# Kernel optimization log

Hardware: AMD Instinct MI355X
Metric: run time of the kernel (lower is better)

The kernel has to match this reference:

```python
import jax, jax.numpy as jnp
import numpy as np

D_MODEL = 1024
NHEAD = 16
HEAD_DIM = D_MODEL // NHEAD
EPS = 1e-5


def _layer_norm(x, gamma, beta):
    mu = jnp.mean(x, axis=-1, keepdims=True)
    var = jnp.mean(jnp.square(x - mu), axis=-1, keepdims=True)
    return (x - mu) * jax.lax.rsqrt(var + EPS) * gamma + beta


def setup_inputs() -> dict:
    key = jax.random.key(0)
    ks = jax.random.split(key, 8)
    s = 1.0 / np.sqrt(D_MODEL)
    return {
        "x": jax.random.normal(ks[0], (4, 2048, D_MODEL), dtype=jnp.float32),
        "Wq": jax.random.uniform(ks[1], (D_MODEL, D_MODEL), jnp.float32, -s, s),
        "Wk": jax.random.uniform(ks[2], (D_MODEL, D_MODEL), jnp.float32, -s, s),
        "Wv": jax.random.uniform(ks[3], (D_MODEL, D_MODEL), jnp.float32, -s, s),
        "ln1_g": jnp.ones((D_MODEL,), jnp.float32),
        "ln1_b": jnp.zeros((D_MODEL,), jnp.float32),
        "ln2_g": jnp.ones((D_MODEL,), jnp.float32),
        "ln2_b": jnp.zeros((D_MODEL,), jnp.float32),
        "W1": jax.random.uniform(ks[4], (D_MODEL, D_MODEL), jnp.float32, -s, s),
        "b1": jax.random.uniform(ks[5], (D_MODEL,), jnp.float32, -s, s),
        "W2": jax.random.uniform(ks[6], (D_MODEL, D_MODEL), jnp.float32, -s, s),
        "b2": jax.random.uniform(ks[7], (D_MODEL,), jnp.float32, -s, s),
    }


def reference(x, Wq, Wk, Wv, ln1_g, ln1_b, ln2_g, ln2_b, W1, b1, W2, b2):
    B, S, D = x.shape
    temperature = jnp.sqrt(jnp.asarray(D_MODEL / NHEAD, x.dtype))
    xn = _layer_norm(x, ln1_g, ln1_b)
    # torch Linear: y = x @ W.T (weights are [out, in], no bias for q/k/v)
    q = (xn @ Wq.T).reshape(B, S, NHEAD, HEAD_DIM)
    k = (xn @ Wk.T).reshape(B, S, NHEAD, HEAD_DIM)
    v = (xn @ Wv.T).reshape(B, S, NHEAD, HEAD_DIM)
    scores = jnp.einsum("bqhd,bkhd->bhqk", q, k) / temperature  # [B,H,S,S]
    causal = jnp.tril(jnp.ones((S, S), dtype=bool))
    scores = jnp.where(causal, scores, jnp.asarray(-jnp.inf, scores.dtype))
    attn = jax.nn.softmax(scores, axis=-1)
    att_out = jnp.einsum("bhqk,bkhd->bqhd", attn, v).reshape(B, S, D)
    xt = x + att_out
    xt2 = _layer_norm(xt, ln2_g, ln2_b)
    ffn = jax.nn.relu(xt2 @ W1.T + b1) @ W2.T + b2  # dropout=0 -> identity
    return xt + ffn
```

## Files before the change

### kernel.cpp

```cpp
#include <hip/hip_runtime.h>
#include <hip/hip_bf16.h>

typedef unsigned short u16;
typedef unsigned int u32;
typedef __attribute__((ext_vector_type(8))) __bf16 bf16x8;
typedef __attribute__((ext_vector_type(4))) float f32x4;
typedef __attribute__((ext_vector_type(8))) unsigned short ushort8v;
typedef __attribute__((ext_vector_type(4))) unsigned short u16x4;
typedef __attribute__((ext_vector_type(2))) unsigned int u32x2;

#define DEV __device__ __forceinline__
#define AS1 __attribute__((address_space(1)))
#define AS3 __attribute__((address_space(3)))

DEV u16 f2bf(float f) {
    union { float f; unsigned int i; } u; u.f = f;
    unsigned int x = u.i;
    unsigned int r = (x + 0x7fffu + ((x >> 16) & 1u)) >> 16;
    return (u16)r;
}
DEV float bf2f(u16 h) {
    union { unsigned int i; float f; } u; u.i = ((unsigned int)h) << 16;
    return u.f;
}
DEV u32 cvt_pk_bf16(float lo, float hi) {
    u32 r;
    asm("v_cvt_pk_bf16_f32 %0, %1, %2" : "=v"(r) : "v"(lo), "v"(hi));
    return r;
}

__global__ __launch_bounds__(256) void cvt_w(
    const float* __restrict__ wq, const float* __restrict__ wk,
    const float* __restrict__ wv, const float* __restrict__ w1,
    const float* __restrict__ w2, u16* __restrict__ dst)
{
    const int i = (blockIdx.x * 256 + threadIdx.x) * 4;
    if (i >= (1 << 20)) return;
    auto conv4 = [](float4 a) {
        u16x4 r; r[0] = f2bf(a.x); r[1] = f2bf(a.y); r[2] = f2bf(a.z); r[3] = f2bf(a.w);
        return r;
    };
    *(u16x4*)(dst + i)               = conv4(*(const float4*)(wq + i));
    *(u16x4*)(dst + (1 << 20) + i)   = conv4(*(const float4*)(wk + i));
    *(u16x4*)(dst + (2 << 20) + i)   = conv4(*(const float4*)(wv + i));
    *(u16x4*)(dst + (3 << 20) + i)   = conv4(*(const float4*)(w1 + i));
    *(u16x4*)(dst + (4 << 20) + i)   = conv4(*(const float4*)(w2 + i));
}

template<bool ADD>
__global__ __launch_bounds__(256) void ln_kernel(
    const float* __restrict__ xin, const u16* __restrict__ addbf,
    const float* __restrict__ g, const float* __restrict__ be,
    float* __restrict__ xt_out, u16* __restrict__ y_bf)
{
    const int row = blockIdx.x;
    const int tid = threadIdx.x;
    const size_t base = (size_t)row * 1024 + tid * 4;

    float4 xv = *(const float4*)(xin + base);
    float v[4] = {xv.x, xv.y, xv.z, xv.w};
    if (ADD) {
        u16x4 a = *(const u16x4*)(addbf + base);
        v[0] += bf2f(a[0]); v[1] += bf2f(a[1]); v[2] += bf2f(a[2]); v[3] += bf2f(a[3]);
        float4 o; o.x = v[0]; o.y = v[1]; o.z = v[2]; o.w = v[3];
        *(float4*)(xt_out + base) = o;
    }
    float s = 0.f, ss = 0.f;
    #pragma unroll
    for (int j = 0; j < 4; ++j) { s += v[j]; ss += v[j] * v[j]; }
    #pragma unroll
    for (int o = 32; o > 0; o >>= 1) { s += __shfl_xor(s, o); ss += __shfl_xor(ss, o); }
    __shared__ float red[8];
    const int w = tid >> 6;
    if ((tid & 63) == 0) { red[w * 2] = s; red[w * 2 + 1] = ss; }
    __syncthreads();
    s  = red[0] + red[2] + red[4] + red[6];
    ss = red[1] + red[3] + red[5] + red[7];
    const float mu = s * (1.0f / 1024.0f);
    const float var = ss * (1.0f / 1024.0f) - mu * mu;
    const float rstd = rsqrtf(var + 1e-5f);

    const int col = tid * 4;
    float4 gv = *(const float4*)(g + col);
    float4 bv = *(const float4*)(be + col);
    u16x4 o4;
    o4[0] = f2bf((v[0] - mu) * rstd * gv.x + bv.x);
    o4[1] = f2bf((v[1] - mu) * rstd * gv.y + bv.y);
    o4[2] = f2bf((v[2] - mu) * rstd * gv.z + bv.z);
    o4[3] = f2bf((v[3] - mu) * rstd * gv.w + bv.w);
    *(u16x4*)(y_bf + base) = o4;
}

template<int EPI>
__global__ __launch_bounds__(256, 2) void gemm_bt(
    const u16* __restrict__ A, const u16* __restrict__ Bt,
    void* __restrict__ Cout, const float* __restrict__ bias,
    const float* __restrict__ resid, int M, int N, int K)
{
    __shared__ u16 As[2 * 128 * 32];
    __shared__ u16 Bs[2 * 128 * 32];
    const int tid = threadIdx.x;
    const int l = tid & 63;
    const int w = tid >> 6;
    const int wm = w >> 1, wn = w & 1;
    const int fr = l & 15, fc = l >> 4;
    const size_t rowA0 = (size_t)blockIdx.x * 128;
    const size_t rowB0 = (size_t)blockIdx.y * 128;

    f32x4 acc[4][4] = {};
    const int ldoff = fr * 32 + fc * 8;

    const int nkt = K >> 6;
    for (int kt = 0; kt < nkt; ++kt) {
        __syncthreads();
        const int k0 = kt << 6;
        #pragma unroll
        for (int q = 0; q < 4; ++q) {
            const int row = (q & 1) * 64 + w * 16 + (l >> 2);
            const int kk  = (q >> 1) * 32 + (l & 3) * 8;
            const u16* ga = A  + (rowA0 + row) * K + k0 + kk;
            const u16* gb = Bt + (rowB0 + row) * K + k0 + kk;
            u16* da = As + q * 2048 + w * 512;
            u16* db = Bs + q * 2048 + w * 512;
            __builtin_amdgcn_global_load_lds((const AS1 void*)ga, (AS3 void*)da, 16, 0, 0);
            __builtin_amdgcn_global_load_lds((const AS1 void*)gb, (AS3 void*)db, 16, 0, 0);
        }
        __syncthreads();
        #pragma unroll
        for (int ks = 0; ks < 2; ++ks) {
            const u16* as_p = As + ks * 4096;
            const u16* bs_p = Bs + ks * 4096;
            bf16x8 af[4], bfv[4];
            #pragma unroll
            for (int m = 0; m < 4; ++m)
                af[m] = *(const bf16x8*)(as_p + (wm * 64 + m * 16) * 32 + ldoff);
            #pragma unroll
            for (int n = 0; n < 4; ++n)
                bfv[n] = *(const bf16x8*)(bs_p + (wn * 64 + n * 16) * 32 + ldoff);
            #pragma unroll
            for (int m = 0; m < 4; ++m)
                #pragma unroll
                for (int n = 0; n < 4; ++n)
                    acc[m][n] = __builtin_amdgcn_mfma_f32_16x16x32_bf16(
                        af[m], bfv[n], acc[m][n], 0, 0, 0);
        }
    }

    const int r0 = (int)rowA0 + wm * 64;
    const int c0 = (int)rowB0 + wn * 64;
    #pragma unroll
    for (int m = 0; m < 4; ++m) {
        #pragma unroll
        for (int n = 0; n < 4; ++n) {
            const int row = r0 + m * 16 + fc * 4;
            const int col = c0 + n * 16 + fr;
            #pragma unroll
            for (int j = 0; j < 4; ++j) {
                float v = acc[m][n][j];
                if constexpr (EPI == 0) {
                    const int rowj = row + j;
                    const int which = col >> 10;
                    const int hh = (col >> 6) & 15;
                    const int dd = col & 63;
                    const size_t dst = (size_t)which * 8388608 +
                        ((((size_t)(rowj >> 11) * 16 + hh) * 2048 + (rowj & 2047)) * 64 + dd);
                    ((u16*)Cout)[dst] = f2bf(v);
                } else if constexpr (EPI == 1) {
                    const size_t idx = (size_t)(row + j) * N + col;
                    v += bias[col];
                    v = fmaxf(v, 0.0f);
                    ((u16*)Cout)[idx] = f2bf(v);
                } else {
                    const size_t idx = (size_t)(row + j) * N + col;
                    v += bias[col] + resid[idx];
                    ((float*)Cout)[idx] = v;
                }
            }
        }
    }
}

__global__ __launch_bounds__(256, 4) void attn_fwd(
    const u16* __restrict__ Qh, const u16* __restrict__ Kh,
    const u16* __restrict__ Vh, u16* __restrict__ attout)
{
    __shared__ u16 Ks[2][64 * 64];
    __shared__ u16 Vt[2][64 * 64];
    __shared__ u16 Pw[4 * 16 * 64];

    const int bid = blockIdx.x;
    const int pair = (bid >> 3) & 15;
    const int g = (bid & 7) + 8 * (bid >> 7);
    const int h = g & 15, b = g >> 4;

    const int tid = threadIdx.x, l = tid & 63, w = tid >> 6;
    const int fr = l & 15, fc = l >> 4;
    const int hb = b * 16 + h;
    const size_t head = (size_t)hb << 17;
    const u16* kb_g = Kh + head;
    const u16* vb_g = Vh + head;
    u16* pw = Pw + w * 1024;

    const int sw = (fr & 7) << 3;
    const int col0 = (fc * 8) ^ sw;
    const int col1 = col0 ^ 32;

    const int krow0 = w * 16 + (l >> 3);
    const int kdsw  = ((l & 7) * 8) ^ ((l >> 3) << 3);

    const int kr = tid >> 2;
    const int kc0 = (tid & 3) * 16;

    const float qs = 0.125f * 1.44269504f;

    bf16x8 onesv;
    #pragma unroll
    for (int j = 0; j < 8; ++j) onesv[j] = (__bf16)1.0f;

    #pragma unroll 1
    for (int half = 0; half < 2; ++half) {
        const int qt = half ? 31 - pair : pair;
        const int qbase = qt * 64 + w * 16;
        const int qg = qbase + fr;

        const u16* qp = Qh + head + (size_t)(qbase + fr) * 64 + fc * 8;
        bf16x8 qf0 = *(const bf16x8*)qp;
        bf16x8 qf1 = *(const bf16x8*)(qp + 32);
        #pragma unroll
        for (int j = 0; j < 8; ++j) {
            qf0[j] = (__bf16)((float)qf0[j] * qs);
            qf1[j] = (__bf16)((float)qf1[j] * qs);
        }

        f32x4 acc_o[4] = {};
        float m_run = -3.0e38f;
        float l_run[4] = {0.f, 0.f, 0.f, 0.f};

        const int nkt = qt + 1;
        int cur = 0;

        #pragma unroll
        for (int i = 0; i < 2; ++i) {
            const int row = krow0 + i * 8;
            __builtin_amdgcn_global_load_lds(
                (const AS1 void*)(kb_g + (size_t)row * 64 + kdsw),
                (AS3 void*)(&Ks[0][0] + (w * 16 + i * 8) * 64), 16, 0, 0);
        }
        __builtin_amdgcn_sched_barrier(0);
        {
            ushort8v v0a = *(const ushort8v*)(vb_g + (size_t)kr * 64 + kc0);
            ushort8v v0b = *(const ushort8v*)(vb_g + (size_t)kr * 64 + kc0 + 8);
            #pragma unroll
            for (int j = 0; j < 8; ++j) {
                const int d0 = kc0 + j, d1 = kc0 + 8 + j;
                Vt[0][d0 * 64 + (kr ^ ((d0 & 7) << 3) ^ ((d0 >> 4) << 4))] = v0a[j];
                Vt[0][d1 * 64 + (kr ^ ((d1 & 7) << 3) ^ ((d1 >> 4) << 4))] = v0b[j];
            }
        }
        ushort8v vA, vB;
        if (nkt > 1) {
            vA = *(const ushort8v*)(vb_g + (size_t)(64 + kr) * 64 + kc0);
            vB = *(const ushort8v*)(vb_g + (size_t)(64 + kr) * 64 + kc0 + 8);
        }
        __builtin_amdgcn_sched_barrier(0);
        if (nkt > 1) asm volatile("s_waitcnt vmcnt(2)" ::: "memory");
        else         asm volatile("s_waitcnt vmcnt(0)" ::: "memory");
        asm volatile("s_waitcnt lgkmcnt(0)" ::: "memory");
        __builtin_amdgcn_s_barrier();

        #pragma unroll 1
        for (int kt = 0; kt < nkt; ++kt) {
            const int kv0 = kt * 64;
            const bool diag = (kt == qt);
            const u16* ksc = &Ks[cur][0];
            const u16* vtc = &Vt[cur][0];

            if (kt + 1 < nkt) {
                u16* ksn = &Ks[cur ^ 1][0];
                #pragma unroll
                for (int i = 0; i < 2; ++i) {
                    const int row = krow0 + i * 8;
                    __builtin_amdgcn_global_load_lds(
                        (const AS1 void*)(kb_g + (size_t)(kv0 + 64 + row) * 64 + kdsw),
                        (AS3 void*)(ksn + (w * 16 + i * 8) * 64), 16, 0, 0);
                }
            }
            __builtin_amdgcn_sched_barrier(0);

            f32x4 sa[4] = {};
            __builtin_amdgcn_s_setprio(1);
            #pragma unroll
            for (int nb = 0; nb < 4; ++nb) {
                const u16* kb = ksc + (nb * 16 + fr) * 64;
                sa[nb] = __builtin_amdgcn_mfma_f32_16x16x32_bf16(
                    *(const bf16x8*)(kb + col0), qf0, sa[nb], 0, 0, 0);
                sa[nb] = __builtin_amdgcn_mfma_f32_16x16x32_bf16(
                    *(const bf16x8*)(kb + col1), qf1, sa[nb], 0, 0, 0);
            }
            __builtin_amdgcn_s_setprio(0);

            if (diag) {
                #pragma unroll
                for (int nb = 0; nb < 4; ++nb)
                    #pragma unroll
                    for (int j = 0; j < 4; ++j) {
                        const int kg = kv0 + nb * 16 + fc * 4 + j;
                        if (kg > qg) sa[nb][j] = -3.0e38f;
                    }
            }

            float mx = sa[0][0];
            #pragma unroll
            for (int nb = 0; nb < 4; ++nb)
                #pragma unroll
                for (int j = 0; j < 4; ++j)
                    mx = fmaxf(mx, sa[nb][j]);
            mx = fmaxf(mx, __shfl_xor(mx, 16));
            mx = fmaxf(mx, __shfl_xor(mx, 32));

            if (__any(mx > m_run + 8.0f)) {
                const float mn = fmaxf(m_run, mx);
                const float alpha = exp2f(m_run - mn);
                m_run = mn;
                float aj[4];
                #pragma unroll
                for (int j = 0; j < 4; ++j)
                    aj[j] = __shfl(alpha, fc * 4 + j);
                #pragma unroll
                for (int j = 0; j < 4; ++j)
                    l_run[j] *= aj[j];
                #pragma unroll
                for (int db = 0; db < 4; ++db)
                    #pragma unroll
                    for (int j = 0; j < 4; ++j)
                        acc_o[db][j] *= aj[j];
            }

            #pragma unroll
            for (int nb = 0; nb < 4; ++nb)
                #pragma unroll
                for (int j = 0; j < 4; ++j)
                    sa[nb][j] = exp2f(sa[nb][j] - m_run);

            #pragma unroll
            for (int nb = 0; nb < 4; ++nb) {
                u32x2 pkv;
                pkv[0] = cvt_pk_bf16(sa[nb][0], sa[nb][1]);
                pkv[1] = cvt_pk_bf16(sa[nb][2], sa[nb][3]);
                *(u32x2*)(pw + fr * 64 + ((nb * 16 + fc * 4) ^ sw)) = pkv;
            }
            const u16* prd = pw + fr * 64;
            const bf16x8 pf0 = *(const bf16x8*)(prd + col0);
            const bf16x8 pf1 = *(const bf16x8*)(prd + col1);
            f32x4 acc_s = {};
            __builtin_amdgcn_s_setprio(1);
            #pragma unroll
            for (int db = 0; db < 4; ++db) {
                const u16* vb = vtc + (db * 16 + fr) * 64;
                const int vx = db << 4;
                acc_o[db] = __builtin_amdgcn_mfma_f32_16x16x32_bf16(
                    pf0, *(const bf16x8*)(vb + (col0 ^ vx)), acc_o[db], 0, 0, 0);
                acc_o[db] = __builtin_amdgcn_mfma_f32_16x16x32_bf16(
                    pf1, *(const bf16x8*)(vb + (col1 ^ vx)), acc_o[db], 0, 0, 0);
            }
            acc_s = __builtin_amdgcn_mfma_f32_16x16x32_bf16(pf0, onesv, acc_s, 0, 0, 0);
            acc_s = __builtin_amdgcn_mfma_f32_16x16x32_bf16(pf1, onesv, acc_s, 0, 0, 0);
            __builtin_amdgcn_s_setprio(0);
            #pragma unroll
            for (int j = 0; j < 4; ++j)
                l_run[j] += acc_s[j];

            if (kt + 1 < nkt) {
                u16* vtn = &Vt[cur ^ 1][0];
                #pragma unroll
                for (int j = 0; j < 8; ++j) {
                    const int d0 = kc0 + j, d1 = kc0 + 8 + j;
                    vtn[d0 * 64 + (kr ^ ((d0 & 7) << 3) ^ ((d0 >> 4) << 4))] = vA[j];
                    vtn[d1 * 64 + (kr ^ ((d1 & 7) << 3) ^ ((d1 >> 4) << 4))] = vB[j];
                }
            }
            if (kt + 2 < nkt) {
                const u16* vn = vb_g + (size_t)(kv0 + 128 + kr) * 64 + kc0;
                vA = *(const ushort8v*)vn;
                vB = *(const ushort8v*)(vn + 8);
            }
            __builtin_amdgcn_sched_barrier(0);
            if (kt + 1 < nkt) {
                if (kt + 2 < nkt) asm volatile("s_waitcnt vmcnt(2)" ::: "memory");
                else              asm volatile("s_waitcnt vmcnt(0)" ::: "memory");
            }
            asm volatile("s_waitcnt lgkmcnt(0)" ::: "memory");
            __builtin_amdgcn_s_barrier();
            cur ^= 1;
        }

        float inv[4];
        #pragma unroll
        for (int j = 0; j < 4; ++j) inv[j] = 1.0f / l_run[j];
        const size_t bS = (size_t)b * 2048;
        #pragma unroll
        for (int db = 0; db < 4; ++db)
            #pragma unroll
            for (int j = 0; j < 4; ++j)
                attout[(bS + qbase + fc * 4 + j) * 1024 + h * 64 + db * 16 + fr] =
                    f2bf(acc_o[db][j] * inv[j]);
    }
}

extern "C" void kernel_launch(void* const* d_in, const int* in_sizes, int n_in,
                              void* d_out, int out_size, void* d_ws, size_t ws_size,
                              hipStream_t stream)
{
    const float* x    = (const float*)d_in[0];
    const float* Wq   = (const float*)d_in[1];
    const float* Wk   = (const float*)d_in[2];
    const float* Wv   = (const float*)d_in[3];
    const float* ln1g = (const float*)d_in[4];
    const float* ln1b = (const float*)d_in[5];
    const float* ln2g = (const float*)d_in[6];
    const float* ln2b = (const float*)d_in[7];
    const float* W1   = (const float*)d_in[8];
    const float* b1   = (const float*)d_in[9];
    const float* W2   = (const float*)d_in[10];
    const float* b2   = (const float*)d_in[11];

    char* ws = (char*)d_ws;
    u16*   wbf  = (u16*)(ws);
    u16*   xn   = (u16*)(ws + 10485760);
    u16*   qkvb = (u16*)(ws + 27262976);
    u16*   attb = (u16*)(ws + 77594624);
    float* xt   = (float*)(ws + 94371840);

    cvt_w<<<1024, 256, 0, stream>>>(Wq, Wk, Wv, W1, W2, wbf);
    ln_kernel<false><<<8192, 256, 0, stream>>>(x, nullptr, ln1g, ln1b, nullptr, xn);
    gemm_bt<0><<<dim3(64, 24), 256, 0, stream>>>(xn, wbf, qkvb, nullptr, nullptr,
                                                 8192, 3072, 1024);
    attn_fwd<<<1024, 256, 0, stream>>>(qkvb, qkvb + 8388608, qkvb + 16777216, attb);
    ln_kernel<true><<<8192, 256, 0, stream>>>(x, attb, ln2g, ln2b, xt, xn);
    gemm_bt<1><<<dim3(64, 8), 256, 0, stream>>>(xn, wbf + (3 << 20), qkvb, b1, nullptr,
                                                8192, 1024, 1024);
    gemm_bt<2><<<dim3(64, 8), 256, 0, stream>>>(qkvb, wbf + (4 << 20), d_out, b2, xt,
                                                8192, 1024, 1024);
}
```

Before: 227.7 us.

## Enlarge attention query tile to 128 rows with two 16-row sub-tiles per wave

Each attention block now handles 128 query rows (32 per wave, as two 16-row MFMA sub-tiles) instead of 64. Every K/V tile loaded into LDS is therefore reused across twice as many queries, which halves K/V staging traffic and barrier count per query, and the grid shrinks to 512 blocks. Per-wave register use roughly doubles for accumulators, so launch bounds drop to 2 waves per SIMD. The coarser tiles also leave fewer blocks for load balancing, and waves whose rows end before the diagonal sit idle on some iterations.

```diff
diff --git a/kernel.cpp b/kernel.cpp
--- a/kernel.cpp
+++ b/kernel.cpp
@@ -180,17 +180,17 @@
     }
 }
 
-__global__ __launch_bounds__(256, 4) void attn_fwd(
+__global__ __launch_bounds__(256, 2) void attn_fwd(
     const u16* __restrict__ Qh, const u16* __restrict__ Kh,
     const u16* __restrict__ Vh, u16* __restrict__ attout)
 {
     __shared__ u16 Ks[2][64 * 64];
     __shared__ u16 Vt[2][64 * 64];
-    __shared__ u16 Pw[4 * 16 * 64];
+    __shared__ u16 Pw[4][32 * 64];
 
     const int bid = blockIdx.x;
-    const int pair = (bid >> 3) & 15;
-    const int g = (bid & 7) + 8 * (bid >> 7);
+    const int pair = (bid >> 3) & 7;
+    const int g = (bid & 7) + 8 * (bid >> 6);
     const int h = g & 15, b = g >> 4;
 
     const int tid = threadIdx.x, l = tid & 63, w = tid >> 6;
@@ -199,7 +199,7 @@
     const size_t head = (size_t)hb << 17;
     const u16* kb_g = Kh + head;
     const u16* vb_g = Vh + head;
-    u16* pw = Pw + w * 1024;
+    u16* pw = &Pw[w][0];
 
     const int sw = (fr & 7) << 3;
     const int col0 = (fc * 8) ^ sw;
@@ -219,24 +219,27 @@
 
     #pragma unroll 1
     for (int half = 0; half < 2; ++half) {
-        const int qt = half ? 31 - pair : pair;
-        const int qbase = qt * 64 + w * 16;
-        const int qg = qbase + fr;
-
-        const u16* qp = Qh + head + (size_t)(qbase + fr) * 64 + fc * 8;
-        bf16x8 qf0 = *(const bf16x8*)qp;
-        bf16x8 qf1 = *(const bf16x8*)(qp + 32);
-        #pragma unroll
-        for (int j = 0; j < 8; ++j) {
-            qf0[j] = (__bf16)((float)qf0[j] * qs);
-            qf1[j] = (__bf16)((float)qf1[j] * qs);
-        }
-
-        f32x4 acc_o[4] = {};
-        float m_run = -3.0e38f;
-        float l_run[4] = {0.f, 0.f, 0.f, 0.f};
-
-        const int nkt = qt + 1;
+        const int qt = half ? 15 - pair : pair;
+        const int qbw = qt * 128 + w * 32;
+
+        bf16x8 qf[2][2];
+        #pragma unroll
+        for (int qq = 0; qq < 2; ++qq) {
+            const u16* qp = Qh + head + (size_t)(qbw + qq * 16 + fr) * 64 + fc * 8;
+            qf[qq][0] = *(const bf16x8*)qp;
+            qf[qq][1] = *(const bf16x8*)(qp + 32);
+            #pragma unroll
+            for (int j = 0; j < 8; ++j) {
+                qf[qq][0][j] = (__bf16)((float)qf[qq][0][j] * qs);
+                qf[qq][1][j] = (__bf16)((float)qf[qq][1][j] * qs);
+            }
+        }
+
+        f32x4 acc_o[2][4] = {};
+        f32x4 l_run[2] = {};
+        float m_run[2] = {-3.0e38f, -3.0e38f};
+
+        const int nkt = 2 * qt + 2;
         int cur = 0;
 
         #pragma unroll
@@ -258,20 +261,18 @@
             }
         }
         ushort8v vA, vB;
-        if (nkt > 1) {
+        {
             vA = *(const ushort8v*)(vb_g + (size_t)(64 + kr) * 64 + kc0);
             vB = *(const ushort8v*)(vb_g + (size_t)(64 + kr) * 64 + kc0 + 8);
         }
         __builtin_amdgcn_sched_barrier(0);
-        if (nkt > 1) asm volatile("s_waitcnt vmcnt(2)" ::: "memory");
-        else         asm volatile("s_waitcnt vmcnt(0)" ::: "memory");
+        asm volatile("s_waitcnt vmcnt(2)" ::: "memory");
         asm volatile("s_waitcnt lgkmcnt(0)" ::: "memory");
         __builtin_amdgcn_s_barrier();
 
         #pragma unroll 1
         for (int kt = 0; kt < nkt; ++kt) {
             const int kv0 = kt * 64;
-            const bool diag = (kt == qt);
             const u16* ksc = &Ks[cur][0];
             const u16* vtc = &Vt[cur][0];
 
@@ -287,88 +288,124 @@
             }
             __builtin_amdgcn_sched_barrier(0);
 
-            f32x4 sa[4] = {};
-            __builtin_amdgcn_s_setprio(1);
-            #pragma unroll
-            for (int nb = 0; nb < 4; ++nb) {
-                const u16* kb = ksc + (nb * 16 + fr) * 64;
-                sa[nb] = __builtin_amdgcn_mfma_f32_16x16x32_bf16(
-                    *(const bf16x8*)(kb + col0), qf0, sa[nb], 0, 0, 0);
-                sa[nb] = __builtin_amdgcn_mfma_f32_16x16x32_bf16(
-                    *(const bf16x8*)(kb + col1), qf1, sa[nb], 0, 0, 0);
-            }
-            __builtin_amdgcn_s_setprio(0);
-
-            if (diag) {
-                #pragma unroll
-                for (int nb = 0; nb < 4; ++nb)
-                    #pragma unroll
-                    for (int j = 0; j < 4; ++j) {
-                        const int kg = kv0 + nb * 16 + fc * 4 + j;
-                        if (kg > qg) sa[nb][j] = -3.0e38f;
+            if (kv0 <= qbw + 31) {
+                f32x4 sa[2][4] = {};
+                __builtin_amdgcn_s_setprio(1);
+                #pragma unroll
+                for (int nb = 0; nb < 4; ++nb) {
+                    const u16* kb = ksc + (nb * 16 + fr) * 64;
+                    const bf16x8 kf0 = *(const bf16x8*)(kb + col0);
+                    const bf16x8 kf1 = *(const bf16x8*)(kb + col1);
+                    #pragma unroll
+                    for (int qq = 0; qq < 2; ++qq) {
+                        sa[qq][nb] = __builtin_amdgcn_mfma_f32_16x16x32_bf16(
+                            kf0, qf[qq][0], sa[qq][nb], 0, 0, 0);
+                        sa[qq][nb] = __builtin_amdgcn_mfma_f32_16x16x32_bf16(
+                            kf1, qf[qq][1], sa[qq][nb], 0, 0, 0);
                     }
-            }
-
-            float mx = sa[0][0];
-            #pragma unroll
-            for (int nb = 0; nb < 4; ++nb)
-                #pragma unroll
-                for (int j = 0; j < 4; ++j)
-                    mx = fmaxf(mx, sa[nb][j]);
-            mx = fmaxf(mx, __shfl_xor(mx, 16));
-            mx = fmaxf(mx, __shfl_xor(mx, 32));
-
-            if (__any(mx > m_run + 8.0f)) {
-                const float mn = fmaxf(m_run, mx);
-                const float alpha = exp2f(m_run - mn);
-                m_run = mn;
-                float aj[4];
-                #pragma unroll
-                for (int j = 0; j < 4; ++j)
-                    aj[j] = __shfl(alpha, fc * 4 + j);
-                #pragma unroll
-                for (int j = 0; j < 4; ++j)
-                    l_run[j] *= aj[j];
-                #pragma unroll
-                for (int db = 0; db < 4; ++db)
+                }
+                __builtin_amdgcn_s_setprio(0);
+
+                if (kv0 + 64 > qbw) {
+                    #pragma unroll
+                    for (int qq = 0; qq < 2; ++qq) {
+                        const int qg = qbw + qq * 16 + fr;
+                        #pragma unroll
+                        for (int nb = 0; nb < 4; ++nb)
+                            #pragma unroll
+                            for (int j = 0; j < 4; ++j) {
+                                const int kg = kv0 + nb * 16 + fc * 4 + j;
+                                if (kg > qg) sa[qq][nb][j] = -3.0e38f;
+                            }
+                    }
+                }
+
+                float mx[2];
+                #pragma unroll
+                for (int qq = 0; qq < 2; ++qq) {
+                    float m = sa[qq][0][0];
+                    #pragma unroll
+                    for (int nb = 0; nb < 4; ++nb)
+                        #pragma unroll
+                        for (int j = 0; j < 4; ++j)
+                            m = fmaxf(m, sa[qq][nb][j]);
+                    m = fmaxf(m, __shfl_xor(m, 16));
+                    m = fmaxf(m, __shfl_xor(m, 32));
+                    mx[qq] = m;
+                }
+
+                const bool need = (mx[0] > m_run[0] + 8.0f) || (mx[1] > m_run[1] + 8.0f);
+                if (__any(need)) {
+                    #pragma unroll
+                    for (int qq = 0; qq < 2; ++qq) {
+                        const float mn = fmaxf(m_run[qq], mx[qq]);
+                        const float alpha = exp2f(m_run[qq] - mn);
+                        m_run[qq] = mn;
+                        #pragma unroll
+                        for (int j = 0; j < 4; ++j) {
+                            const float aj = __shfl(alpha, fc * 4 + j);
+                            l_run[qq][j] *= aj;
+                            #pragma unroll
+                            for (int db = 0; db < 4; ++db)
+                                acc_o[qq][db][j] *= aj;
+                        }
+                    }
+                }
+
+                #pragma unroll
+                for (int qq = 0; qq < 2; ++qq)
+                    #pragma unroll
+                    for (int nb = 0; nb < 4; ++nb)
+                        #pragma unroll
+                        for (int j = 0; j < 4; ++j)
+                            sa[qq][nb][j] = exp2f(sa[qq][nb][j] - m_run[qq]);
+
+                #pragma unroll
+                for (int qq = 0; qq < 2; ++qq)
+                    #pragma unroll
+                    for (int nb = 0; nb < 4; ++nb) {
+                        u32x2 pkv;
+                        pkv[0] = cvt_pk_bf16(sa[qq][nb][0], sa[qq][nb][1]);
+                        pkv[1] = cvt_pk_bf16(sa[qq][nb][2], sa[qq][nb][3]);
+                        *(u32x2*)(pw + (qq * 16 + fr) * 64 + ((nb * 16 + fc * 4) ^ sw)) = pkv;
+                    }
+                bf16x8 pf[2][2];
+                #pragma unroll
+                for (int qq = 0; qq < 2; ++qq) {
+                    const u16* prd = pw + (qq * 16 + fr) * 64;
+                    pf[qq][0] = *(const bf16x8*)(prd + col0);
+                    pf[qq][1] = *(const bf16x8*)(prd + col1);
+                }
+                f32x4 acc_s[2] = {};
+                __builtin_amdgcn_s_setprio(1);
+                #pragma unroll
+                for (int db = 0; db < 4; ++db) {
+                    const u16* vb = vtc + (db * 16 + fr) * 64;
+                    const int vx = db << 4;
+                    const bf16x8 vf0 = *(const bf16x8*)(vb + (col0 ^ vx));
+                    const bf16x8 vf1 = *(const bf16x8*)(vb + (col1 ^ vx));
+                    #pragma unroll
+                    for (int qq = 0; qq < 2; ++qq) {
+                        acc_o[qq][db] = __builtin_amdgcn_mfma_f32_16x16x32_bf16(
+                            pf[qq][0], vf0, acc_o[qq][db], 0, 0, 0);
+                        acc_o[qq][db] = __builtin_amdgcn_mfma_f32_16x16x32_bf16(
+                            pf[qq][1], vf1, acc_o[qq][db], 0, 0, 0);
+                    }
+                }
+                #pragma unroll
+                for (int qq = 0; qq < 2; ++qq) {
+                    acc_s[qq] = __builtin_amdgcn_mfma_f32_16x16x32_bf16(
+                        pf[qq][0], onesv, acc_s[qq], 0, 0, 0);
+                    acc_s[qq] = __builtin_amdgcn_mfma_f32_16x16x32_bf16(
+                        pf[qq][1], onesv, acc_s[qq], 0, 0, 0);
+                }
+                __builtin_amdgcn_s_setprio(0);
+                #pragma unroll
+                for (int qq = 0; qq < 2; ++qq)
                     #pragma unroll
                     for (int j = 0; j < 4; ++j)
-                        acc_o[db][j] *= aj[j];
-            }
-
-            #pragma unroll
-            for (int nb = 0; nb < 4; ++nb)
-                #pragma unroll
-                for (int j = 0; j < 4; ++j)
-                    sa[nb][j] = exp2f(sa[nb][j] - m_run);
-
-            #pragma unroll
-            for (int nb = 0; nb < 4; ++nb) {
-                u32x2 pkv;
-                pkv[0] = cvt_pk_bf16(sa[nb][0], sa[nb][1]);
-                pkv[1] = cvt_pk_bf16(sa[nb][2], sa[nb][3]);
-                *(u32x2*)(pw + fr * 64 + ((nb * 16 + fc * 4) ^ sw)) = pkv;
-            }
-            const u16* prd = pw + fr * 64;
-            const bf16x8 pf0 = *(const bf16x8*)(prd + col0);
-            const bf16x8 pf1 = *(const bf16x8*)(prd + col1);
-            f32x4 acc_s = {};
-            __builtin_amdgcn_s_setprio(1);
-            #pragma unroll
-            for (int db = 0; db < 4; ++db) {
-                const u16* vb = vtc + (db * 16 + fr) * 64;
-                const int vx = db << 4;
-                acc_o[db] = __builtin_amdgcn_mfma_f32_16x16x32_bf16(
-                    pf0, *(const bf16x8*)(vb + (col0 ^ vx)), acc_o[db], 0, 0, 0);
-                acc_o[db] = __builtin_amdgcn_mfma_f32_16x16x32_bf16(
-                    pf1, *(const bf16x8*)(vb + (col1 ^ vx)), acc_o[db], 0, 0, 0);
-            }
-            acc_s = __builtin_amdgcn_mfma_f32_16x16x32_bf16(pf0, onesv, acc_s, 0, 0, 0);
-            acc_s = __builtin_amdgcn_mfma_f32_16x16x32_bf16(pf1, onesv, acc_s, 0, 0, 0);
-            __builtin_amdgcn_s_setprio(0);
-            #pragma unroll
-            for (int j = 0; j < 4; ++j)
-                l_run[j] += acc_s[j];
+                        l_run[qq][j] += acc_s[qq][j];
+            }
 
             if (kt + 1 < nkt) {
                 u16* vtn = &Vt[cur ^ 1][0];
@@ -394,16 +431,19 @@
             cur ^= 1;
         }
 
-        float inv[4];
-        #pragma unroll
-        for (int j = 0; j < 4; ++j) inv[j] = 1.0f / l_run[j];
         const size_t bS = (size_t)b * 2048;
         #pragma unroll
-        for (int db = 0; db < 4; ++db)
-            #pragma unroll
-            for (int j = 0; j < 4; ++j)
-                attout[(bS + qbase + fc * 4 + j) * 1024 + h * 64 + db * 16 + fr] =
-                    f2bf(acc_o[db][j] * inv[j]);
+        for (int qq = 0; qq < 2; ++qq) {
+            float inv[4];
+            #pragma unroll
+            for (int j = 0; j < 4; ++j) inv[j] = 1.0f / l_run[qq][j];
+            #pragma unroll
+            for (int db = 0; db < 4; ++db)
+                #pragma unroll
+                for (int j = 0; j < 4; ++j)
+                    attout[(bS + qbw + qq * 16 + fc * 4 + j) * 1024 + h * 64 + db * 16 + fr] =
+                        f2bf(acc_o[qq][db][j] * inv[j]);
+        }
     }
 }
 
@@ -435,7 +475,7 @@
     ln_kernel<false><<<8192, 256, 0, stream>>>(x, nullptr, ln1g, ln1b, nullptr, xn);
     gemm_bt<0><<<dim3(64, 24), 256, 0, stream>>>(xn, wbf, qkvb, nullptr, nullptr,
                                                  8192, 3072, 1024);
-    attn_fwd<<<1024, 256, 0, stream>>>(qkvb, qkvb + 8388608, qkvb + 16777216, attb);
+    attn_fwd<<<512, 256, 0, stream>>>(qkvb, qkvb + 8388608, qkvb + 16777216, attb);
     ln_kernel<true><<<8192, 256, 0, stream>>>(x, attb, ln2g, ln2b, xt, xn);
     gemm_bt<1><<<dim3(64, 8), 256, 0, stream>>>(xn, wbf + (3 << 20), qkvb, b1, nullptr,
                                                 8192, 1024, 1024);
```

Result: no change. 228.5 us (+0.3%).

## Write V pre-transposed from QKV GEMM and load it directly into LDS

Applied to the files above, without the earlier changes.

The QKV projection epilogue now stores V in a [head, dim, seq] transposed layout instead of [head, seq, dim]. The attention kernel can then stage V tiles into LDS with the same async global_load_lds path used for K, with no register round-trip or scalar scattered transpose stores, and the V MFMA reads drop their extra XOR swizzle. The cost is strided, uncoalesced 2-byte scattered writes of V in the GEMM epilogue, and a simpler full vmcnt(0) wait each iteration.

```diff
diff --git a/kernel.cpp b/kernel.cpp
--- a/kernel.cpp
+++ b/kernel.cpp
@@ -162,8 +162,13 @@
                     const int which = col >> 10;
                     const int hh = (col >> 6) & 15;
                     const int dd = col & 63;
-                    const size_t dst = (size_t)which * 8388608 +
-                        ((((size_t)(rowj >> 11) * 16 + hh) * 2048 + (rowj & 2047)) * 64 + dd);
+                    const size_t hb = (size_t)(rowj >> 11) * 16 + hh;
+                    const int s = rowj & 2047;
+                    size_t dst;
+                    if (which == 2)
+                        dst = (size_t)2 * 8388608 + (hb * 64 + dd) * 2048 + s;
+                    else
+                        dst = (size_t)which * 8388608 + (hb * 2048 + s) * 64 + dd;
                     ((u16*)Cout)[dst] = f2bf(v);
                 } else if constexpr (EPI == 1) {
                     const size_t idx = (size_t)(row + j) * N + col;
@@ -186,7 +191,7 @@
 {
     __shared__ u16 Ks[2][64 * 64];
     __shared__ u16 Vt[2][64 * 64];
-    __shared__ u16 Pw[4 * 16 * 64];
+    __shared__ u16 Pw[4][16 * 64];
 
     const int bid = blockIdx.x;
     const int pair = (bid >> 3) & 15;
@@ -199,17 +204,14 @@
     const size_t head = (size_t)hb << 17;
     const u16* kb_g = Kh + head;
     const u16* vb_g = Vh + head;
-    u16* pw = Pw + w * 1024;
+    u16* pw = &Pw[w][0];
 
     const int sw = (fr & 7) << 3;
     const int col0 = (fc * 8) ^ sw;
     const int col1 = col0 ^ 32;
 
-    const int krow0 = w * 16 + (l >> 3);
-    const int kdsw  = ((l & 7) * 8) ^ ((l >> 3) << 3);
-
-    const int kr = tid >> 2;
-    const int kc0 = (tid & 3) * 16;
+    const int grow0 = w * 16 + (l >> 3);
+    const int gsw   = ((l & 7) * 8) ^ ((l >> 3) << 3);
 
     const float qs = 0.125f * 1.44269504f;
 
@@ -241,31 +243,16 @@
 
         #pragma unroll
         for (int i = 0; i < 2; ++i) {
-            const int row = krow0 + i * 8;
+            const int row = grow0 + i * 8;
             __builtin_amdgcn_global_load_lds(
-                (const AS1 void*)(kb_g + (size_t)row * 64 + kdsw),
+                (const AS1 void*)(kb_g + (size_t)row * 64 + gsw),
                 (AS3 void*)(&Ks[0][0] + (w * 16 + i * 8) * 64), 16, 0, 0);
+            __builtin_amdgcn_global_load_lds(
+                (const AS1 void*)(vb_g + (size_t)row * 2048 + gsw),
+                (AS3 void*)(&Vt[0][0] + (w * 16 + i * 8) * 64), 16, 0, 0);
         }
         __builtin_amdgcn_sched_barrier(0);
-        {
-            ushort8v v0a = *(const ushort8v*)(vb_g + (size_t)kr * 64 + kc0);
-            ushort8v v0b = *(const ushort8v*)(vb_g + (size_t)kr * 64 + kc0 + 8);
-            #pragma unroll
-            for (int j = 0; j < 8; ++j) {
-                const int d0 = kc0 + j, d1 = kc0 + 8 + j;
-                Vt[0][d0 * 64 + (kr ^ ((d0 & 7) << 3) ^ ((d0 >> 4) << 4))] = v0a[j];
-                Vt[0][d1 * 64 + (kr ^ ((d1 & 7) << 3) ^ ((d1 >> 4) << 4))] = v0b[j];
-            }
-        }
-        ushort8v vA, vB;
-        if (nkt > 1) {
-            vA = *(const ushort8v*)(vb_g + (size_t)(64 + kr) * 64 + kc0);
-            vB = *(const ushort8v*)(vb_g + (size_t)(64 + kr) * 64 + kc0 + 8);
-        }
-        __builtin_amdgcn_sched_barrier(0);
-        if (nkt > 1) asm volatile("s_waitcnt vmcnt(2)" ::: "memory");
-        else         asm volatile("s_waitcnt vmcnt(0)" ::: "memory");
-        asm volatile("s_waitcnt lgkmcnt(0)" ::: "memory");
+        asm volatile("s_waitcnt vmcnt(0)" ::: "memory");
         __builtin_amdgcn_s_barrier();
 
         #pragma unroll 1
@@ -277,12 +264,16 @@
 
             if (kt + 1 < nkt) {
                 u16* ksn = &Ks[cur ^ 1][0];
+                u16* vtn = &Vt[cur ^ 1][0];
                 #pragma unroll
                 for (int i = 0; i < 2; ++i) {
-                    const int row = krow0 + i * 8;
+                    const int row = grow0 + i * 8;
                     __builtin_amdgcn_global_load_lds(
-                        (const AS1 void*)(kb_g + (size_t)(kv0 + 64 + row) * 64 + kdsw),
+                        (const AS1 void*)(kb_g + (size_t)(kv0 + 64 + row) * 64 + gsw),
                         (AS3 void*)(ksn + (w * 16 + i * 8) * 64), 16, 0, 0);
+                    __builtin_amdgcn_global_load_lds(
+                        (const AS1 void*)(vb_g + (size_t)row * 2048 + kv0 + 64 + gsw),
+                        (AS3 void*)(vtn + (w * 16 + i * 8) * 64), 16, 0, 0);
                 }
             }
             __builtin_amdgcn_sched_barrier(0);
@@ -357,11 +348,10 @@
             #pragma unroll
             for (int db = 0; db < 4; ++db) {
                 const u16* vb = vtc + (db * 16 + fr) * 64;
-                const int vx = db << 4;
                 acc_o[db] = __builtin_amdgcn_mfma_f32_16x16x32_bf16(
-                    pf0, *(const bf16x8*)(vb + (col0 ^ vx)), acc_o[db], 0, 0, 0);
+                    pf0, *(const bf16x8*)(vb + col0), acc_o[db], 0, 0, 0);
                 acc_o[db] = __builtin_amdgcn_mfma_f32_16x16x32_bf16(
-                    pf1, *(const bf16x8*)(vb + (col1 ^ vx)), acc_o[db], 0, 0, 0);
+                    pf1, *(const bf16x8*)(vb + col1), acc_o[db], 0, 0, 0);
             }
             acc_s = __builtin_amdgcn_mfma_f32_16x16x32_bf16(pf0, onesv, acc_s, 0, 0, 0);
             acc_s = __builtin_amdgcn_mfma_f32_16x16x32_bf16(pf1, onesv, acc_s, 0, 0, 0);
@@ -370,25 +360,8 @@
             for (int j = 0; j < 4; ++j)
                 l_run[j] += acc_s[j];
 
-            if (kt + 1 < nkt) {
-                u16* vtn = &Vt[cur ^ 1][0];
-                #pragma unroll
-                for (int j = 0; j < 8; ++j) {
-                    const int d0 = kc0 + j, d1 = kc0 + 8 + j;
-                    vtn[d0 * 64 + (kr ^ ((d0 & 7) << 3) ^ ((d0 >> 4) << 4))] = vA[j];
-                    vtn[d1 * 64 + (kr ^ ((d1 & 7) << 3) ^ ((d1 >> 4) << 4))] = vB[j];
-                }
-            }
-            if (kt + 2 < nkt) {
-                const u16* vn = vb_g + (size_t)(kv0 + 128 + kr) * 64 + kc0;
-                vA = *(const ushort8v*)vn;
-                vB = *(const ushort8v*)(vn + 8);
-            }
             __builtin_amdgcn_sched_barrier(0);
-            if (kt + 1 < nkt) {
-                if (kt + 2 < nkt) asm volatile("s_waitcnt vmcnt(2)" ::: "memory");
-                else              asm volatile("s_waitcnt vmcnt(0)" ::: "memory");
-            }
+            asm volatile("s_waitcnt vmcnt(0)" ::: "memory");
             asm volatile("s_waitcnt lgkmcnt(0)" ::: "memory");
             __builtin_amdgcn_s_barrier();
             cur ^= 1;
```

After: 234.4 us. 2.9% more time.
